# Kernel tuning notes

Hardware: AMD Instinct MI355X
Metric: run time of the kernel (lower is better)

The kernel has to match this reference:

```python
import jax, jax.numpy as jnp
import numpy as np

BATCH, SEQ = 4, 2048
D_MODEL, D_STATE, D_CONV, HEADDIM = 512, 128, 4, 64
D_INNER = 1024          # expand * d_model
NHEADS = 16             # d_inner / headdim
CONV_DIM = D_INNER + 2 * D_STATE   # 1280 (ngroups=1)
D_IN_PROJ = 2 * D_INNER + 2 * D_STATE + NHEADS  # 2320


def setup_inputs() -> dict:
    key = jax.random.key(0)
    ks = jax.random.split(key, 7)
    x = jax.random.normal(ks[0], (BATCH, SEQ, D_MODEL), jnp.float32)
    norm_weight = jnp.ones((D_MODEL,), jnp.float32)
    in_proj_w = jax.random.normal(ks[1], (D_IN_PROJ, D_MODEL), jnp.float32) * 0.02
    conv_w = jax.random.normal(ks[2], (CONV_DIM, 1, D_CONV), jnp.float32) * 0.2
    conv_b = jnp.zeros((CONV_DIM,), jnp.float32)
    dt_bias = jax.random.normal(ks[3], (NHEADS,), jnp.float32) * 0.1
    A_log = jnp.log(jax.random.uniform(ks[4], (NHEADS,), jnp.float32, 1.0, 16.0))
    D_param = jnp.ones((NHEADS,), jnp.float32)
    gated_norm_weight = jnp.ones((D_INNER,), jnp.float32)
    out_proj_w = jax.random.normal(ks[5], (D_MODEL, D_INNER), jnp.float32) * 0.02
    return dict(x=x, norm_weight=norm_weight, in_proj_w=in_proj_w, conv_w=conv_w,
                conv_b=conv_b, dt_bias=dt_bias, A_log=A_log, D_param=D_param,
                gated_norm_weight=gated_norm_weight, out_proj_w=out_proj_w)


def _rmsnorm(x, w, eps):
    return w * (x * jax.lax.rsqrt(jnp.mean(x * x, axis=-1, keepdims=True) + eps))


def _mamba2_forward(x, norm_weight, in_proj_w, conv_w, conv_b, dt_bias,
                    A_log, D_param, gated_norm_weight, out_proj_w):
    b, l, _ = x.shape
    u = _rmsnorm(x, norm_weight, 1e-6)                       # pre-norm (eps=1e-6)
    zxbcdt = u @ in_proj_w.T                                 # (b,l,2320)
    z = zxbcdt[..., :D_INNER]                                # gate
    xBC = zxbcdt[..., D_INNER:D_INNER + CONV_DIM]            # (b,l,1280)
    dt = zxbcdt[..., D_INNER + CONV_DIM:]                    # (b,l,nheads)
    dt = jax.nn.softplus(dt + dt_bias)

    # causal depthwise conv1d over time + SiLU
    conv = jax.lax.conv_general_dilated(
        xBC.transpose(0, 2, 1), conv_w, window_strides=(1,),
        padding=[(D_CONV - 1, 0)], feature_group_count=CONV_DIM,
        dimension_numbers=('NCH', 'OIH', 'NCH'))
    xBC = jax.nn.silu((conv + conv_b[None, :, None]).transpose(0, 2, 1))

    xs = xBC[..., :D_INNER].reshape(b, l, NHEADS, HEADDIM)   # (b,l,h,p)
    Bmat = xBC[..., D_INNER:D_INNER + D_STATE]               # (b,l,n)
    Cmat = xBC[..., D_INNER + D_STATE:]                      # (b,l,n)

    A = -jnp.exp(A_log)                                      # (h,)
    dA = jnp.exp(dt * A)                                     # (b,l,h)
    dtx = dt[..., None] * xs                                 # (b,l,h,p)

    def step(h, inp):
        dA_t, dtx_t, B_t, C_t = inp                          # (b,h),(b,h,p),(b,n),(b,n)
        h = h * dA_t[..., None, None] + dtx_t[..., None] * B_t[:, None, None, :]
        y = jnp.einsum('bhpn,bn->bhp', h, C_t)
        return h, y

    h0 = jnp.zeros((b, NHEADS, HEADDIM, D_STATE), x.dtype)
    _, ys = jax.lax.scan(step, h0, (dA.transpose(1, 0, 2), dtx.transpose(1, 0, 2, 3),
                                    Bmat.transpose(1, 0, 2), Cmat.transpose(1, 0, 2)))
    y = ys.transpose(1, 0, 2, 3) + xs * D_param[None, None, :, None]  # D skip
    y = y.reshape(b, l, D_INNER)

    y = _rmsnorm(y * jax.nn.silu(z), gated_norm_weight, 1e-5)  # RMSNormGated (eps=1e-5)
    return x + y @ out_proj_w.T                                # residual


def reference(x, norm_weight, in_proj_w, conv_w, conv_b, dt_bias,
              A_log, D_param, gated_norm_weight, out_proj_w):
    return _mamba2_forward(x, norm_weight, in_proj_w, conv_w, conv_b, dt_bias,
                           A_log, D_param, gated_norm_weight, out_proj_w)
```

## Files before the change

kernel.cpp:

```cpp
#include <hip/hip_runtime.h>
#include <cstdint>
#include <cstddef>

#define B_ 4
#define L_ 2048
#define DMODEL 512
#define DINNER 1024
#define DSTATE 128
#define NH 16
#define HD 64
#define CONVDIM 1280
#define NPROJ 2320
#define NPAD 2432
#define ML (B_*L_)
#define Q_ 64
#define NCH 32

typedef __bf16 bf16x8 __attribute__((ext_vector_type(8)));
typedef float f32x4 __attribute__((ext_vector_type(4)));
typedef float f32x16 __attribute__((ext_vector_type(16)));

__device__ __forceinline__ float bf2f(ushort u) {
  union { unsigned int i; float f; } v; v.i = ((unsigned int)u) << 16; return v.f;
}
__device__ __forceinline__ ushort f2bf(float f) {
  union { float f; unsigned int i; } v; v.f = f;
  unsigned int u = v.i;
  unsigned int r = (u + 0x7fffu + ((u >> 16) & 1u)) >> 16;
  return (ushort)r;
}
__device__ __forceinline__ float siluf(float x) { return x / (1.f + __expf(-x)); }

__device__ __forceinline__ void gl_lds16(const void* g, void* l) {
  __builtin_amdgcn_global_load_lds(
      (const __attribute__((address_space(1))) unsigned int*)g,
      (__attribute__((address_space(3))) unsigned int*)l,
      16, 0, 0);
}

__global__ __launch_bounds__(256) void k_cvt(const float* __restrict__ wi, const float* __restrict__ wo,
                                             const float* __restrict__ gw,
                                             ushort* __restrict__ oi, ushort* __restrict__ oo) {
  int idx = blockIdx.x * 256 + threadIdx.x;
  const int n1 = NPAD * DMODEL;
  if (idx < n1) {
    int n = idx / DMODEL, k = idx % DMODEL;
    oi[idx] = f2bf((n < NPROJ) ? wi[(size_t)n * DMODEL + k] : 0.f);
  } else {
    int j = idx - n1;
    if (j < DMODEL * DINNER) oo[j] = f2bf(wo[j] * gw[j & (DINNER - 1)]);
  }
}

__global__ __launch_bounds__(256) void k_rmsnorm(const float* __restrict__ x, const float* __restrict__ w,
                                                 ushort* __restrict__ u) {
  int row = blockIdx.x * 4 + (threadIdx.x >> 6);
  int lane = threadIdx.x & 63;
  const float* xr = x + (size_t)row * DMODEL + lane * 8;
  float4 a = *(const float4*)xr;
  float4 b = *(const float4*)(xr + 4);
  float ss = a.x*a.x + a.y*a.y + a.z*a.z + a.w*a.w + b.x*b.x + b.y*b.y + b.z*b.z + b.w*b.w;
  ss += __shfl_xor(ss, 1);  ss += __shfl_xor(ss, 2);  ss += __shfl_xor(ss, 4);
  ss += __shfl_xor(ss, 8);  ss += __shfl_xor(ss, 16); ss += __shfl_xor(ss, 32);
  float sc = rsqrtf(ss * (1.f / DMODEL) + 1e-6f);
  const float* wr = w + lane * 8;
  float4 wa = *(const float4*)wr;
  float4 wb = *(const float4*)(wr + 4);
  union { ushort s[8]; int4 v; } o;
  o.s[0] = f2bf(a.x * wa.x * sc); o.s[1] = f2bf(a.y * wa.y * sc);
  o.s[2] = f2bf(a.z * wa.z * sc); o.s[3] = f2bf(a.w * wa.w * sc);
  o.s[4] = f2bf(b.x * wb.x * sc); o.s[5] = f2bf(b.y * wb.y * sc);
  o.s[6] = f2bf(b.z * wb.z * sc); o.s[7] = f2bf(b.w * wb.w * sc);
  *(int4*)(u + (size_t)row * DMODEL + lane * 8) = o.v;
}

template <int EPI, int BM, int BN, int MR, int NR>
__global__ __launch_bounds__(256) void gemm_bt(const ushort* __restrict__ A, const ushort* __restrict__ Bm,
                                               void* __restrict__ Cout, const float* __restrict__ resid,
                                               const float* __restrict__ rescale,
                                               int M, int N, int K, int gx) {
  constexpr int WM = MR * 32, WN = NR * 32;
  constexpr int WAVES_N = BN / WN;
  constexpr int CH_A = BM / 8, CH_B = BN / 8;
  constexpr int PER_A = CH_A / 4, PER_B = CH_B / 4;
  constexpr int SL = PER_A + PER_B;
  __shared__ __align__(16) ushort lA[2][BM * 64];
  __shared__ __align__(16) ushort lB[2][BN * 64];
  const int nwg = gridDim.x;
  const int cpx = nwg >> 3;
  const int bid = blockIdx.x;
  const int swz = (bid & 7) * cpx + (bid >> 3);
  const int n0 = (swz % gx) * BN, m0 = (swz / gx) * BM;
  const int t = threadIdx.x;
  const int wave = t >> 6, lane = t & 63;
  const int wr = wave / WAVES_N, wc = wave % WAVES_N;
  const int r3 = lane >> 3;
  const int ce = (((lane & 7) ^ r3) << 3);
  const int nt = K >> 6;
  f32x16 acc[MR][NR] = {};
  auto stage = [&](int buf, int k0) {
#pragma unroll
    for (int i = 0; i < PER_A; ++i) {
      int chunk = wave * PER_A + i;
      int row = chunk * 8 + r3;
      gl_lds16(A + (size_t)(m0 + row) * K + k0 + ce, (char*)&lA[buf][0] + chunk * 1024);
    }
#pragma unroll
    for (int i = 0; i < PER_B; ++i) {
      int chunk = wave * PER_B + i;
      int row = chunk * 8 + r3;
      gl_lds16(Bm + (size_t)(n0 + row) * K + k0 + ce, (char*)&lB[buf][0] + chunk * 1024);
    }
  };
  stage(0, 0);
  const int rsel = lane & 31;
  const int khi = (lane >> 5) << 3;
  const int kswz = (lane & 7) << 3;
  for (int kt = 0; kt < nt; ++kt) {
    const int cur = kt & 1;
    if (kt + 1 < nt) {
      stage(cur ^ 1, (kt + 1) << 6);
      if constexpr (SL == 8) asm volatile("s_waitcnt vmcnt(8)" ::: "memory");
      else if constexpr (SL == 6) asm volatile("s_waitcnt vmcnt(6)" ::: "memory");
      else asm volatile("s_waitcnt vmcnt(0)" ::: "memory");
    } else {
      asm volatile("s_waitcnt vmcnt(0)" ::: "memory");
    }
    __builtin_amdgcn_s_barrier();
#pragma unroll
    for (int kk = 0; kk < 64; kk += 16) {
      const int kcol = (kk + khi) ^ kswz;
      bf16x8 af[MR], bfr[NR];
#pragma unroll
      for (int m = 0; m < MR; ++m)
        af[m] = *reinterpret_cast<const bf16x8*>(&lA[cur][(wr * WM + m * 32 + rsel) * 64 + kcol]);
#pragma unroll
      for (int n = 0; n < NR; ++n)
        bfr[n] = *reinterpret_cast<const bf16x8*>(&lB[cur][(wc * WN + n * 32 + rsel) * 64 + kcol]);
#pragma unroll
      for (int m = 0; m < MR; ++m)
#pragma unroll
        for (int n = 0; n < NR; ++n)
          acc[m][n] = __builtin_amdgcn_mfma_f32_32x32x16_bf16(af[m], bfr[n], acc[m][n], 0, 0, 0);
    }
    __builtin_amdgcn_s_barrier();
  }
  const int coln = lane & 31;
  const int rbase = (lane >> 5) << 2;
#pragma unroll
  for (int m = 0; m < MR; ++m) {
#pragma unroll
    for (int n = 0; n < NR; ++n) {
      int gm0 = m0 + wr * WM + m * 32 + rbase;
      int gn = n0 + wc * WN + n * 32 + coln;
#pragma unroll
      for (int r = 0; r < 16; ++r) {
        int gm = gm0 + (r & 3) + 8 * (r >> 2);
        float v = acc[m][n][r];
        if (EPI == 0) {
          ((ushort*)Cout)[(size_t)gm * N + gn] = f2bf(v);
        } else {
          ((float*)Cout)[(size_t)gm * N + gn] = v * rescale[gm] + resid[(size_t)gm * N + gn];
        }
      }
    }
  }
}

__global__ __launch_bounds__(256) void k_dtcum(const ushort* __restrict__ zx, const float* __restrict__ dt_bias,
                                               const float* __restrict__ A_log, float* __restrict__ dtb,
                                               float* __restrict__ acum, float* __restrict__ rs) {
  int flat = blockIdx.x * 256 + threadIdx.x;
  if (flat < ML) rs[flat] = 0.f;
  int gid = blockIdx.x * 4 + (threadIdx.x >> 6);
  int lane = threadIdx.x & 63;
  int c = gid & 31, h = (gid >> 5) & 15, b = gid >> 9;
  int row = b * L_ + c * Q_ + lane;
  float raw = bf2f(zx[(size_t)row * NPAD + DINNER + CONVDIM + h]) + dt_bias[h];
  float dtv = raw > 20.f ? raw : log1pf(expf(raw));
  dtb[(size_t)row * NH + h] = dtv;
  float a = dtv * (-__expf(A_log[h]));
#pragma unroll
  for (int d = 1; d < 64; d <<= 1) {
    float o = __shfl_up(a, d);
    if (lane >= d) a += o;
  }
  acum[(size_t)row * NH + h] = a;
}

__global__ __launch_bounds__(256) void k_conv(const ushort* __restrict__ zx, const float* __restrict__ cw,
                                              const float* __restrict__ cb, ushort* __restrict__ out) {
  int t = blockIdx.x * 256 + threadIdx.x;
  int cg = t % 160;
  int rb = t / 160;
  int c0 = cg * 8;
  int l0 = (rb & 255) * 8;
  int b = rb >> 8;
  float w0[8], w1[8], w2[8], w3[8], bias[8];
#pragma unroll
  for (int j = 0; j < 8; ++j) {
    float4 wv = *(const float4*)(cw + (c0 + j) * 4);
    w0[j] = wv.x; w1[j] = wv.y; w2[j] = wv.z; w3[j] = wv.w;
    bias[j] = cb[c0 + j];
  }
  const ushort* base = zx + (size_t)(b * L_ + l0) * NPAD + DINNER + c0;
  ushort* ob = out + (size_t)(b * L_ + l0) * CONVDIM + c0;
  union U8 { int4 v; ushort s[8]; };
  float h0[8], h1[8], h2[8];
  if (l0 >= 3) {
    U8 a, bb, cc;
    a.v  = *(const int4*)(base - 3 * NPAD);
    bb.v = *(const int4*)(base - 2 * NPAD);
    cc.v = *(const int4*)(base - 1 * NPAD);
#pragma unroll
    for (int j = 0; j < 8; ++j) { h0[j] = bf2f(a.s[j]); h1[j] = bf2f(bb.s[j]); h2[j] = bf2f(cc.s[j]); }
  } else {
#pragma unroll
    for (int j = 0; j < 8; ++j) { h0[j] = 0.f; h1[j] = 0.f; h2[j] = 0.f; }
  }
#pragma unroll
  for (int i = 0; i < 8; ++i) {
    U8 xv, ov;
    xv.v = *(const int4*)(base + (size_t)i * NPAD);
#pragma unroll
    for (int j = 0; j < 8; ++j) {
      float xc = bf2f(xv.s[j]);
      float v = w0[j] * h0[j] + w1[j] * h1[j] + w2[j] * h2[j] + w3[j] * xc + bias[j];
      ov.s[j] = f2bf(siluf(v));
      h0[j] = h1[j]; h1[j] = h2[j]; h2[j] = xc;
    }
    *(int4*)(ob + (size_t)i * CONVDIM) = ov.v;
  }
}

__global__ __launch_bounds__(256) void k_state(const ushort* __restrict__ xbc, const float* __restrict__ dtb,
                                               const float* __restrict__ acum, ushort* __restrict__ Sbuf) {
  __shared__ __align__(16) ushort sBTW[128 * 72];
  __shared__ __align__(16) ushort sXT[64 * 72];
  __shared__ float sDt[64], sCum[64];
  const int blk = blockIdx.x;
  const int c = blk & 31, h = (blk >> 5) & 15, b = blk >> 9;
  const int row0 = b * L_ + c * Q_;
  const int tid = threadIdx.x;
  const int wave = tid >> 6, lane = tid & 63;
  if (tid < 64) {
    sDt[tid]  = dtb[(size_t)(row0 + tid) * NH + h];
    sCum[tid] = acum[(size_t)(row0 + tid) * NH + h];
  }
  __syncthreads();
  const float T = sCum[63];
#pragma unroll
  for (int i = 0; i < 4; ++i) {
    int idx = i * 256 + tid;
    int r = idx >> 4, n8 = (idx & 15) * 8;
    union { int4 v; ushort s[8]; } bv;
    bv.v = *(const int4*)(xbc + (size_t)(row0 + r) * CONVDIM + DINNER + n8);
    float w = sDt[r] * __expf(T - sCum[r]);
#pragma unroll
    for (int j = 0; j < 8; ++j)
      sBTW[(n8 + j) * 72 + r] = f2bf(bf2f(bv.s[j]) * w);
  }
#pragma unroll
  for (int i = 0; i < 2; ++i) {
    int idx = i * 256 + tid;
    int r = idx >> 3, p8 = (idx & 7) * 8;
    union { int4 v; ushort s[8]; } xv;
    xv.v = *(const int4*)(xbc + (size_t)(row0 + r) * CONVDIM + h * HD + p8);
#pragma unroll
    for (int j = 0; j < 8; ++j) sXT[(p8 + j) * 72 + r] = xv.s[j];
  }
  __syncthreads();
  const int rsel = lane & 15;
  const int t0 = wave * 16;
  f32x4 sa[8] = {};
#pragma unroll
  for (int k0 = 0; k0 < 64; k0 += 32) {
    int ksel = k0 + ((lane >> 4) << 3);
    bf16x8 af = *(const bf16x8*)&sXT[(t0 + rsel) * 72 + ksel];
#pragma unroll
    for (int n = 0; n < 8; ++n) {
      bf16x8 bf_ = *(const bf16x8*)&sBTW[(n * 16 + rsel) * 72 + ksel];
      sa[n] = __builtin_amdgcn_mfma_f32_16x16x32_bf16(af, bf_, sa[n], 0, 0, 0);
    }
  }
  ushort* Sp = Sbuf + (size_t)((b * NH + h) * NCH + c) * (HD * DSTATE);
  int prow = t0 + ((lane >> 4) << 2);
#pragma unroll
  for (int n = 0; n < 8; ++n) {
    int nc = n * 16 + (lane & 15);
#pragma unroll
    for (int r = 0; r < 4; ++r)
      Sp[(prow + r) * DSTATE + nc] = f2bf(sa[n][r]);
  }
}

__global__ __launch_bounds__(256) void k_scan2(ushort* __restrict__ Sbuf, const float* __restrict__ acum) {
  const int blk = blockIdx.x;
  const int ps = blk & 3, bh = blk >> 2;
  const int b = bh >> 4, h = bh & 15;
  const int off = ps * 2048 + threadIdx.x * 8;
  ushort* base = Sbuf + (size_t)bh * NCH * (HD * DSTATE) + off;
  float alphas[NCH];
#pragma unroll
  for (int c = 0; c < NCH; ++c)
    alphas[c] = __expf(acum[(size_t)(b * L_ + c * Q_ + 63) * NH + h]);
  union U8 { int4 v; ushort s[8]; };
  U8 pf[4];
#pragma unroll
  for (int i = 0; i < 4; ++i) pf[i].v = *(const int4*)(base + (size_t)i * (HD * DSTATE));
  float hreg[8] = {};
  U8 hv;
#pragma unroll
  for (int c = 0; c < NCH; ++c) {
    U8 cur = pf[c & 3];
    if (c + 4 < NCH) pf[c & 3].v = *(const int4*)(base + (size_t)(c + 4) * (HD * DSTATE));
#pragma unroll
    for (int i = 0; i < 8; ++i) hv.s[i] = f2bf(hreg[i]);
    *(int4*)(base + (size_t)c * (HD * DSTATE)) = hv.v;
#pragma unroll
    for (int i = 0; i < 8; ++i) hreg[i] = fmaf(alphas[c], hreg[i], bf2f(cur.s[i]));
  }
}

__global__ __launch_bounds__(256) void k_y(const ushort* __restrict__ xbc, const ushort* __restrict__ zx,
                                           const ushort* __restrict__ Hin,
                                           const float* __restrict__ dtb, const float* __restrict__ acum,
                                           const float* __restrict__ Dp, ushort* __restrict__ yb,
                                           float* __restrict__ rs) {
  __shared__ __align__(16) ushort sC[64 * 136];
  __shared__ __align__(16) ushort sB[64 * 136];
  __shared__ __align__(16) ushort sH[64 * 136];
  __shared__ __align__(16) ushort sXT[64 * 72];
  __shared__ float sDt[64], sCum[64];
  const int blk = blockIdx.x;
  const int c = blk & 31, h = (blk >> 5) & 15, b = blk >> 9;
  const int row0 = b * L_ + c * Q_;
  const int tid = threadIdx.x;
  const int wave = tid >> 6, lane = tid & 63;
  if (tid < 64) {
    sDt[tid]  = dtb[(size_t)(row0 + tid) * NH + h];
    sCum[tid] = acum[(size_t)(row0 + tid) * NH + h];
  }
  const ushort* Hp = Hin + (size_t)((b * NH + h) * NCH + c) * (HD * DSTATE);
#pragma unroll
  for (int i = 0; i < 4; ++i) {
    int idx = i * 256 + tid;
    int r = idx >> 4, n8 = (idx & 15) * 8;
    const ushort* src = xbc + (size_t)(row0 + r) * CONVDIM + DINNER + n8;
    *(int4*)&sB[r * 136 + n8] = *(const int4*)src;
    *(int4*)&sC[r * 136 + n8] = *(const int4*)(src + DSTATE);
    *(int4*)&sH[r * 136 + n8] = *(const int4*)(Hp + (size_t)r * DSTATE + n8);
  }
#pragma unroll
  for (int i = 0; i < 2; ++i) {
    int idx = i * 256 + tid;
    int r = idx >> 3, p8 = (idx & 7) * 8;
    union { int4 v; ushort s[8]; } xv;
    xv.v = *(const int4*)(xbc + (size_t)(row0 + r) * CONVDIM + h * HD + p8);
#pragma unroll
    for (int j = 0; j < 8; ++j) sXT[(p8 + j) * 72 + r] = xv.s[j];
  }
  __syncthreads();
  const int rsel = lane & 15;
  const int t0 = wave * 16;
  f32x4 g[4] = {};
  f32x4 y2[4] = {};
#pragma unroll
  for (int k0 = 0; k0 < 128; k0 += 32) {
    int ksel = k0 + ((lane >> 4) << 3);
    bf16x8 af = *(const bf16x8*)&sC[(t0 + rsel) * 136 + ksel];
#pragma unroll
    for (int s = 0; s < 4; ++s) {
      bf16x8 bf_ = *(const bf16x8*)&sB[(s * 16 + rsel) * 136 + ksel];
      g[s] = __builtin_amdgcn_mfma_f32_16x16x32_bf16(af, bf_, g[s], 0, 0, 0);
      bf16x8 hf = *(const bf16x8*)&sH[(s * 16 + rsel) * 136 + ksel];
      y2[s] = __builtin_amdgcn_mfma_f32_16x16x32_bf16(af, hf, y2[s], 0, 0, 0);
    }
  }
  {
    int trow = t0 + ((lane >> 4) << 2);
#pragma unroll
    for (int s = 0; s < 4; ++s) {
      int sc_ = s * 16 + (lane & 15);
      float dts = sDt[sc_], cums = sCum[sc_];
#pragma unroll
      for (int r = 0; r < 4; ++r) {
        int t2 = trow + r;
        float mv = (sc_ <= t2) ? g[s][r] * dts * __expf(sCum[t2] - cums) : 0.f;
        sC[t2 * 136 + sc_] = f2bf(mv);
      }
    }
  }
  f32x4 yi[4] = {};
#pragma unroll
  for (int k0 = 0; k0 < 64; k0 += 32) {
    int ksel = k0 + ((lane >> 4) << 3);
    bf16x8 af = *(const bf16x8*)&sC[(t0 + rsel) * 136 + ksel];
#pragma unroll
    for (int p = 0; p < 4; ++p) {
      bf16x8 bf_ = *(const bf16x8*)&sXT[(p * 16 + rsel) * 72 + ksel];
      yi[p] = __builtin_amdgcn_mfma_f32_16x16x32_bf16(af, bf_, yi[p], 0, 0, 0);
    }
  }
  const float Dh = Dp[h];
  int trow = t0 + ((lane >> 4) << 2);
  float rsum[4] = {0.f, 0.f, 0.f, 0.f};
#pragma unroll
  for (int p = 0; p < 4; ++p) {
    int pc = p * 16 + (lane & 15);
#pragma unroll
    for (int r = 0; r < 4; ++r) {
      int t2 = trow + r;
      float v = yi[p][r] + __expf(sCum[t2]) * y2[p][r] + Dh * bf2f(sXT[pc * 72 + t2]);
      float zf = bf2f(zx[(size_t)(row0 + t2) * NPAD + h * HD + pc]);
      float gg = v * siluf(zf);
      rsum[r] += gg * gg;
      yb[(size_t)(row0 + t2) * DINNER + h * HD + pc] = f2bf(gg);
    }
  }
#pragma unroll
  for (int r = 0; r < 4; ++r) {
    float s = rsum[r];
    s += __shfl_xor(s, 1); s += __shfl_xor(s, 2); s += __shfl_xor(s, 4); s += __shfl_xor(s, 8);
    if ((lane & 15) == 0) atomicAdd(&rs[row0 + trow + r], s);
  }
}

__global__ __launch_bounds__(256) void k_scale(float* __restrict__ rs) {
  int i = blockIdx.x * 256 + threadIdx.x;
  rs[i] = rsqrtf(rs[i] * (1.f / DINNER) + 1e-5f);
}

extern "C" void kernel_launch(void* const* d_in, const int* in_sizes, int n_in,
                              void* d_out, int out_size, void* d_ws, size_t ws_size,
                              hipStream_t stream) {
  const float* x         = (const float*)d_in[0];
  const float* norm_w    = (const float*)d_in[1];
  const float* in_proj_w = (const float*)d_in[2];
  const float* conv_w    = (const float*)d_in[3];
  const float* conv_b    = (const float*)d_in[4];
  const float* dt_bias   = (const float*)d_in[5];
  const float* A_log     = (const float*)d_in[6];
  const float* D_param   = (const float*)d_in[7];
  const float* gnw       = (const float*)d_in[8];
  const float* out_proj_w= (const float*)d_in[9];

  char* ws = (char*)d_ws;
  ushort* u      = (ushort*)(ws + 0);
  float*  rs     = (float*)(ws + 0);
  ushort* Wb     = (ushort*)(ws + 8388608);
  ushort* Woutb  = (ushort*)(ws + 10878976);
  float*  dtb    = (float*)(ws + 11927552);
  float*  acum   = (float*)(ws + 12451840);
  ushort* zx     = (ushort*)(ws + 12976128);
  ushort* convo  = (ushort*)(ws + 52822016);
  ushort* yb     = (ushort*)(ws + 73793536);
  ushort* Sbuf   = (ushort*)(ws + 90570752);

  k_cvt<<<(NPAD * DMODEL + DMODEL * DINNER + 255) / 256, 256, 0, stream>>>(in_proj_w, out_proj_w, gnw, Wb, Woutb);
  k_rmsnorm<<<ML / 4, 256, 0, stream>>>(x, norm_w, u);
  gemm_bt<0, 128, 128, 2, 2><<<(NPAD / 128) * (ML / 128), 256, 0, stream>>>(u, Wb, (void*)zx, nullptr, nullptr, ML, NPAD, DMODEL, NPAD / 128);
  k_dtcum<<<512, 256, 0, stream>>>(zx, dt_bias, A_log, dtb, acum, rs);
  k_conv<<<640, 256, 0, stream>>>(zx, conv_w, conv_b, convo);
  k_state<<<2048, 256, 0, stream>>>(convo, dtb, acum, Sbuf);
  k_scan2<<<256, 256, 0, stream>>>(Sbuf, acum);
  k_y<<<2048, 256, 0, stream>>>(convo, zx, Sbuf, dtb, acum, D_param, yb, rs);
  k_scale<<<ML / 256, 256, 0, stream>>>(rs);
  gemm_bt<3, 128, 64, 2, 1><<<(DMODEL / 64) * (ML / 128), 256, 0, stream>>>(yb, Woutb, d_out, x, rs, ML, DMODEL, DINNER, DMODEL / 64);
}
```

Baseline: 149.3 us.

## Emit transposed X and B from conv to remove LDS transposes in state/y kernels

```diff
diff --git a/kernel.cpp b/kernel.cpp
--- a/kernel.cpp
+++ b/kernel.cpp
@@ -189,109 +189,118 @@
 }
 
 __global__ __launch_bounds__(256) void k_conv(const ushort* __restrict__ zx, const float* __restrict__ cw,
-                                              const float* __restrict__ cb, ushort* __restrict__ out) {
+                                              const float* __restrict__ cb, ushort* __restrict__ convBC,
+                                              ushort* __restrict__ XT, ushort* __restrict__ BT) {
   int t = blockIdx.x * 256 + threadIdx.x;
-  int cg = t % 160;
-  int rb = t / 160;
-  int c0 = cg * 8;
-  int l0 = (rb & 255) * 8;
-  int b = rb >> 8;
-  float w0[8], w1[8], w2[8], w3[8], bias[8];
-#pragma unroll
-  for (int j = 0; j < 8; ++j) {
-    float4 wv = *(const float4*)(cw + (c0 + j) * 4);
-    w0[j] = wv.x; w1[j] = wv.y; w2[j] = wv.z; w3[j] = wv.w;
-    bias[j] = cb[c0 + j];
-  }
-  const ushort* base = zx + (size_t)(b * L_ + l0) * NPAD + DINNER + c0;
-  ushort* ob = out + (size_t)(b * L_ + l0) * CONVDIM + c0;
-  union U8 { int4 v; ushort s[8]; };
-  float h0[8], h1[8], h2[8];
+  int ch = t % CONVDIM;
+  int rb = t / CONVDIM;
+  int lb = rb & 63, b = rb >> 6;
+  int l0 = lb * 32;
+  float4 wv = *(const float4*)(cw + ch * 4);
+  float bias = cb[ch];
+  const size_t rowb = (size_t)b * L_;
+  const ushort* ip = zx + (rowb + l0) * NPAD + DINNER + ch;
+  float x0 = 0.f, x1 = 0.f, x2 = 0.f;
   if (l0 >= 3) {
-    U8 a, bb, cc;
-    a.v  = *(const int4*)(base - 3 * NPAD);
-    bb.v = *(const int4*)(base - 2 * NPAD);
-    cc.v = *(const int4*)(base - 1 * NPAD);
-#pragma unroll
-    for (int j = 0; j < 8; ++j) { h0[j] = bf2f(a.s[j]); h1[j] = bf2f(bb.s[j]); h2[j] = bf2f(cc.s[j]); }
+    x0 = bf2f(ip[-3 * NPAD]); x1 = bf2f(ip[-2 * NPAD]); x2 = bf2f(ip[-1 * NPAD]);
+  }
+  ushort* xdst = nullptr; ushort* bdst = nullptr; ushort* bcdst = nullptr;
+  if (ch < DINNER) {
+    int h = ch >> 6, p = ch & 63;
+    xdst = XT + ((size_t)(b * NH + h) * HD + p) * L_ + l0;
+  } else if (ch < DINNER + DSTATE) {
+    int n = ch - DINNER;
+    bdst = BT + ((size_t)b * DSTATE + n) * L_ + l0;
+    bcdst = convBC + (rowb + l0) * 256 + n;
   } else {
-#pragma unroll
-    for (int j = 0; j < 8; ++j) { h0[j] = 0.f; h1[j] = 0.f; h2[j] = 0.f; }
-  }
-#pragma unroll
-  for (int i = 0; i < 8; ++i) {
-    U8 xv, ov;
-    xv.v = *(const int4*)(base + (size_t)i * NPAD);
-#pragma unroll
-    for (int j = 0; j < 8; ++j) {
-      float xc = bf2f(xv.s[j]);
-      float v = w0[j] * h0[j] + w1[j] * h1[j] + w2[j] * h2[j] + w3[j] * xc + bias[j];
-      ov.s[j] = f2bf(siluf(v));
-      h0[j] = h1[j]; h1[j] = h2[j]; h2[j] = xc;
-    }
-    *(int4*)(ob + (size_t)i * CONVDIM) = ov.v;
-  }
-}
-
-__global__ __launch_bounds__(256) void k_state(const ushort* __restrict__ xbc, const float* __restrict__ dtb,
-                                               const float* __restrict__ acum, ushort* __restrict__ Sbuf) {
-  __shared__ __align__(16) ushort sBTW[128 * 72];
-  __shared__ __align__(16) ushort sXT[64 * 72];
-  __shared__ float sDt[64], sCum[64];
+    int n = ch - DINNER - DSTATE;
+    bcdst = convBC + (rowb + l0) * 256 + 128 + n;
+  }
+  union U8 { int4 v; ushort s[8]; } buf;
+#pragma unroll
+  for (int i = 0; i < 32; ++i) {
+    float x3 = bf2f(ip[(size_t)i * NPAD]);
+    float v = wv.x * x0 + wv.y * x1 + wv.z * x2 + wv.w * x3 + bias;
+    ushort sv = f2bf(siluf(v));
+    x0 = x1; x1 = x2; x2 = x3;
+    buf.s[i & 7] = sv;
+    if (bcdst) bcdst[(size_t)i * 256] = sv;
+    if ((i & 7) == 7) {
+      if (xdst) *(int4*)(xdst + (i & ~7)) = buf.v;
+      if (bdst) *(int4*)(bdst + (i & ~7)) = buf.v;
+    }
+  }
+}
+
+__global__ __launch_bounds__(256) void k_state(const ushort* __restrict__ XT, const ushort* __restrict__ BT,
+                                               const float* __restrict__ dtb, const float* __restrict__ acum,
+                                               ushort* __restrict__ Sbuf) {
+  __shared__ __align__(16) ushort sXW[64 * 72];
+  __shared__ __align__(16) ushort sBT[128 * 64];
+  __shared__ float sDt[64], sCum[64], sW[64];
   const int blk = blockIdx.x;
   const int c = blk & 31, h = (blk >> 5) & 15, b = blk >> 9;
   const int row0 = b * L_ + c * Q_;
   const int tid = threadIdx.x;
   const int wave = tid >> 6, lane = tid & 63;
+  const int r3 = lane >> 3;
+  const int ce = (((lane & 7) ^ r3) << 3);
+  const ushort* btb = BT + (size_t)b * DSTATE * L_ + c * Q_;
+#pragma unroll
+  for (int i = 0; i < 4; ++i) {
+    int chunk = wave * 4 + i;
+    int row = chunk * 8 + r3;
+    gl_lds16(btb + (size_t)row * L_ + ce, (char*)sBT + chunk * 1024);
+  }
   if (tid < 64) {
     sDt[tid]  = dtb[(size_t)(row0 + tid) * NH + h];
     sCum[tid] = acum[(size_t)(row0 + tid) * NH + h];
   }
   __syncthreads();
-  const float T = sCum[63];
-#pragma unroll
-  for (int i = 0; i < 4; ++i) {
-    int idx = i * 256 + tid;
-    int r = idx >> 4, n8 = (idx & 15) * 8;
-    union { int4 v; ushort s[8]; } bv;
-    bv.v = *(const int4*)(xbc + (size_t)(row0 + r) * CONVDIM + DINNER + n8);
-    float w = sDt[r] * __expf(T - sCum[r]);
-#pragma unroll
-    for (int j = 0; j < 8; ++j)
-      sBTW[(n8 + j) * 72 + r] = f2bf(bf2f(bv.s[j]) * w);
-  }
-#pragma unroll
-  for (int i = 0; i < 2; ++i) {
-    int idx = i * 256 + tid;
-    int r = idx >> 3, p8 = (idx & 7) * 8;
-    union { int4 v; ushort s[8]; } xv;
-    xv.v = *(const int4*)(xbc + (size_t)(row0 + r) * CONVDIM + h * HD + p8);
-#pragma unroll
-    for (int j = 0; j < 8; ++j) sXT[(p8 + j) * 72 + r] = xv.s[j];
-  }
+  if (tid < 64) sW[tid] = sDt[tid] * __expf(sCum[63] - sCum[tid]);
   __syncthreads();
-  const int rsel = lane & 15;
-  const int t0 = wave * 16;
-  f32x4 sa[8] = {};
-#pragma unroll
-  for (int k0 = 0; k0 < 64; k0 += 32) {
-    int ksel = k0 + ((lane >> 4) << 3);
-    bf16x8 af = *(const bf16x8*)&sXT[(t0 + rsel) * 72 + ksel];
-#pragma unroll
-    for (int n = 0; n < 8; ++n) {
-      bf16x8 bf_ = *(const bf16x8*)&sBTW[(n * 16 + rsel) * 72 + ksel];
-      sa[n] = __builtin_amdgcn_mfma_f32_16x16x32_bf16(af, bf_, sa[n], 0, 0, 0);
+  const ushort* xtb = XT + (size_t)(b * NH + h) * HD * L_ + c * Q_;
+#pragma unroll
+  for (int j = 0; j < 2; ++j) {
+    int u = tid * 2 + j;
+    int p = u >> 3, t8 = (u & 7) * 8;
+    union { int4 v; ushort s[8]; } xv, ov;
+    xv.v = *(const int4*)(xtb + (size_t)p * L_ + t8);
+    float4 wa = *(const float4*)&sW[t8];
+    float4 wb2 = *(const float4*)&sW[t8 + 4];
+    ov.s[0] = f2bf(bf2f(xv.s[0]) * wa.x); ov.s[1] = f2bf(bf2f(xv.s[1]) * wa.y);
+    ov.s[2] = f2bf(bf2f(xv.s[2]) * wa.z); ov.s[3] = f2bf(bf2f(xv.s[3]) * wa.w);
+    ov.s[4] = f2bf(bf2f(xv.s[4]) * wb2.x); ov.s[5] = f2bf(bf2f(xv.s[5]) * wb2.y);
+    ov.s[6] = f2bf(bf2f(xv.s[6]) * wb2.z); ov.s[7] = f2bf(bf2f(xv.s[7]) * wb2.w);
+    *(int4*)&sXW[p * 72 + t8] = ov.v;
+  }
+  asm volatile("s_waitcnt vmcnt(0)" ::: "memory");
+  __syncthreads();
+  const int rsel = lane & 31;
+  const int khi = (lane >> 5) << 3;
+  const int kswz = (lane & 7) << 3;
+  f32x16 acc[2] = {};
+#pragma unroll
+  for (int kk = 0; kk < 64; kk += 16) {
+    const int kA = kk + khi;
+    const int kB = kA ^ kswz;
+    bf16x8 bfrg = *(const bf16x8*)&sBT[(wave * 32 + rsel) * 64 + kB];
+#pragma unroll
+    for (int m = 0; m < 2; ++m) {
+      bf16x8 afrg = *(const bf16x8*)&sXW[(m * 32 + rsel) * 72 + kA];
+      acc[m] = __builtin_amdgcn_mfma_f32_32x32x16_bf16(afrg, bfrg, acc[m], 0, 0, 0);
     }
   }
   ushort* Sp = Sbuf + (size_t)((b * NH + h) * NCH + c) * (HD * DSTATE);
-  int prow = t0 + ((lane >> 4) << 2);
-#pragma unroll
-  for (int n = 0; n < 8; ++n) {
-    int nc = n * 16 + (lane & 15);
-#pragma unroll
-    for (int r = 0; r < 4; ++r)
-      Sp[(prow + r) * DSTATE + nc] = f2bf(sa[n][r]);
-  }
+  const int ncol = wave * 32 + (lane & 31);
+  const int rbase = (lane >> 5) << 2;
+#pragma unroll
+  for (int m = 0; m < 2; ++m)
+#pragma unroll
+    for (int r = 0; r < 16; ++r) {
+      int prow = m * 32 + rbase + (r & 3) + 8 * (r >> 2);
+      Sp[prow * DSTATE + ncol] = f2bf(acc[m][r]);
+    }
 }
 
 __global__ __launch_bounds__(256) void k_scan2(ushort* __restrict__ Sbuf, const float* __restrict__ acum) {
@@ -322,21 +331,30 @@
   }
 }
 
-__global__ __launch_bounds__(256) void k_y(const ushort* __restrict__ xbc, const ushort* __restrict__ zx,
-                                           const ushort* __restrict__ Hin,
+__global__ __launch_bounds__(256) void k_y(const ushort* __restrict__ convBC, const ushort* __restrict__ XT,
+                                           const ushort* __restrict__ zx, const ushort* __restrict__ Hin,
                                            const float* __restrict__ dtb, const float* __restrict__ acum,
                                            const float* __restrict__ Dp, ushort* __restrict__ yb,
                                            float* __restrict__ rs) {
   __shared__ __align__(16) ushort sC[64 * 136];
   __shared__ __align__(16) ushort sB[64 * 136];
   __shared__ __align__(16) ushort sH[64 * 136];
-  __shared__ __align__(16) ushort sXT[64 * 72];
+  __shared__ __align__(16) ushort sXS[64 * 64];
   __shared__ float sDt[64], sCum[64];
   const int blk = blockIdx.x;
   const int c = blk & 31, h = (blk >> 5) & 15, b = blk >> 9;
   const int row0 = b * L_ + c * Q_;
   const int tid = threadIdx.x;
   const int wave = tid >> 6, lane = tid & 63;
+  const int r3 = lane >> 3;
+  const int ce = (((lane & 7) ^ r3) << 3);
+  const ushort* xtb = XT + (size_t)(b * NH + h) * HD * L_ + c * Q_;
+#pragma unroll
+  for (int i = 0; i < 2; ++i) {
+    int chunk = wave * 2 + i;
+    int row = chunk * 8 + r3;
+    gl_lds16(xtb + (size_t)row * L_ + ce, (char*)sXS + chunk * 1024);
+  }
   if (tid < 64) {
     sDt[tid]  = dtb[(size_t)(row0 + tid) * NH + h];
     sCum[tid] = acum[(size_t)(row0 + tid) * NH + h];
@@ -346,23 +364,16 @@
   for (int i = 0; i < 4; ++i) {
     int idx = i * 256 + tid;
     int r = idx >> 4, n8 = (idx & 15) * 8;
-    const ushort* src = xbc + (size_t)(row0 + r) * CONVDIM + DINNER + n8;
+    const ushort* src = convBC + (size_t)(row0 + r) * 256 + n8;
     *(int4*)&sB[r * 136 + n8] = *(const int4*)src;
-    *(int4*)&sC[r * 136 + n8] = *(const int4*)(src + DSTATE);
+    *(int4*)&sC[r * 136 + n8] = *(const int4*)(src + 128);
     *(int4*)&sH[r * 136 + n8] = *(const int4*)(Hp + (size_t)r * DSTATE + n8);
   }
-#pragma unroll
-  for (int i = 0; i < 2; ++i) {
-    int idx = i * 256 + tid;
-    int r = idx >> 3, p8 = (idx & 7) * 8;
-    union { int4 v; ushort s[8]; } xv;
-    xv.v = *(const int4*)(xbc + (size_t)(row0 + r) * CONVDIM + h * HD + p8);
-#pragma unroll
-    for (int j = 0; j < 8; ++j) sXT[(p8 + j) * 72 + r] = xv.s[j];
-  }
+  asm volatile("s_waitcnt vmcnt(0)" ::: "memory");
   __syncthreads();
   const int rsel = lane & 15;
   const int t0 = wave * 16;
+  const int kswz = (lane & 7) << 3;
   f32x4 g[4] = {};
   f32x4 y2[4] = {};
 #pragma unroll
@@ -398,7 +409,7 @@
     bf16x8 af = *(const bf16x8*)&sC[(t0 + rsel) * 136 + ksel];
 #pragma unroll
     for (int p = 0; p < 4; ++p) {
-      bf16x8 bf_ = *(const bf16x8*)&sXT[(p * 16 + rsel) * 72 + ksel];
+      bf16x8 bf_ = *(const bf16x8*)&sXS[(p * 16 + rsel) * 64 + (ksel ^ kswz)];
       yi[p] = __builtin_amdgcn_mfma_f32_16x16x32_bf16(af, bf_, yi[p], 0, 0, 0);
     }
   }
@@ -411,7 +422,8 @@
 #pragma unroll
     for (int r = 0; r < 4; ++r) {
       int t2 = trow + r;
-      float v = yi[p][r] + __expf(sCum[t2]) * y2[p][r] + Dh * bf2f(sXT[pc * 72 + t2]);
+      float xval = bf2f(sXS[pc * 64 + (t2 ^ ((pc & 7) << 3))]);
+      float v = yi[p][r] + __expf(sCum[t2]) * y2[p][r] + Dh * xval;
       float zf = bf2f(zx[(size_t)(row0 + t2) * NPAD + h * HD + pc]);
       float gg = v * siluf(zf);
       rsum[r] += gg * gg;
@@ -447,24 +459,26 @@
 
   char* ws = (char*)d_ws;
   ushort* u      = (ushort*)(ws + 0);
-  float*  rs     = (float*)(ws + 0);
+  ushort* convBC = (ushort*)(ws + 0);
+  ushort* BT     = (ushort*)(ws + 4194304);
+  float*  rs     = (float*)(ws + 6291456);
   ushort* Wb     = (ushort*)(ws + 8388608);
   ushort* Woutb  = (ushort*)(ws + 10878976);
   float*  dtb    = (float*)(ws + 11927552);
   float*  acum   = (float*)(ws + 12451840);
   ushort* zx     = (ushort*)(ws + 12976128);
-  ushort* convo  = (ushort*)(ws + 52822016);
-  ushort* yb     = (ushort*)(ws + 73793536);
-  ushort* Sbuf   = (ushort*)(ws + 90570752);
+  ushort* XT     = (ushort*)(ws + 52822016);
+  ushort* yb     = (ushort*)(ws + 69599232);
+  ushort* Sbuf   = (ushort*)(ws + 86376448);
 
   k_cvt<<<(NPAD * DMODEL + DMODEL * DINNER + 255) / 256, 256, 0, stream>>>(in_proj_w, out_proj_w, gnw, Wb, Woutb);
   k_rmsnorm<<<ML / 4, 256, 0, stream>>>(x, norm_w, u);
   gemm_bt<0, 128, 128, 2, 2><<<(NPAD / 128) * (ML / 128), 256, 0, stream>>>(u, Wb, (void*)zx, nullptr, nullptr, ML, NPAD, DMODEL, NPAD / 128);
   k_dtcum<<<512, 256, 0, stream>>>(zx, dt_bias, A_log, dtb, acum, rs);
-  k_conv<<<640, 256, 0, stream>>>(zx, conv_w, conv_b, convo);
-  k_state<<<2048, 256, 0, stream>>>(convo, dtb, acum, Sbuf);
+  k_conv<<<CONVDIM, 256, 0, stream>>>(zx, conv_w, conv_b, convBC, XT, BT);
+  k_state<<<2048, 256, 0, stream>>>(XT, BT, dtb, acum, Sbuf);
   k_scan2<<<256, 256, 0, stream>>>(Sbuf, acum);
-  k_y<<<2048, 256, 0, stream>>>(convo, zx, Sbuf, dtb, acum, D_param, yb, rs);
+  k_y<<<2048, 256, 0, stream>>>(convBC, XT, zx, Sbuf, dtb, acum, D_param, yb, rs);
   k_scale<<<ML / 256, 256, 0, stream>>>(rs);
   gemm_bt<3, 128, 64, 2, 1><<<(DMODEL / 64) * (ML / 128), 256, 0, stream>>>(yb, Woutb, d_out, x, rs, ML, DMODEL, DINNER, DMODEL / 64);
 }
```

New measurement: 146.5 us. Within noise of the previous version (-1.9%).
